# Kernel tuning notes

Measured on AMD Instinct MI355X. Metric: run time of the kernel, lower is better.

Reference implementation:

```python
import jax, jax.numpy as jnp
import numpy as np

NEG_BIG = -9e15
ALPHA = 0.2  # leakyrelu negative slope

N, F_IN, F_OUT = 8192, 512, 64


def setup_inputs() -> dict:
    key = jax.random.key(0)
    k1, k2, k3, k4 = jax.random.split(key, 4)
    input = jax.random.normal(k1, (N, F_IN), dtype=jnp.float32)
    adj = jax.random.randint(k2, (N, N), 0, 2, dtype=jnp.int32)
    W = jax.random.normal(k3, (F_IN, F_OUT), dtype=jnp.float32) * 0.05
    a = jax.random.normal(k4, (2 * F_OUT, 1), dtype=jnp.float32) * 0.1
    return {"input": input, "adj": adj, "W": W, "a": a}


def reference(input, adj, W, a):
    # h: [N, F_out]
    h = input @ W
    # The original builds a_input[i,j] = concat(h_i, h_j) and dots with a.
    # Decompose: e_ij = leakyrelu(h_i @ a_src + h_j @ a_dst) -- identical math,
    # avoids the N*N*2F intermediate.
    a_src = a[:F_OUT, 0]  # [F_out]
    a_dst = a[F_OUT:, 0]  # [F_out]
    s_src = h @ a_src     # [N]
    s_dst = h @ a_dst     # [N]
    e = jax.nn.leaky_relu(s_src[:, None] + s_dst[None, :], negative_slope=ALPHA)  # [N, N]
    masked = jnp.where(adj > 0, e, jnp.float32(NEG_BIG))
    attention = jax.nn.softmax(masked, axis=1)  # dropout omitted (eval mode)
    h_prime = attention @ h  # [N, F_out]
    return jax.nn.elu(h_prime)  # concat=True
```

## Files before the change

### kernel.cpp

```cpp
#include <hip/hip_runtime.h>
#include <hip/hip_bf16.h>

namespace {
constexpr int kN    = 8192;
constexpr int kFin  = 512;
constexpr int kFout = 64;
constexpr float kAlpha = 0.2f;
constexpr int kJSplit = 4;
constexpr int kJLen   = kN / kJSplit;
constexpr int kChunks = kJLen / 128;

using bf16x8 = __attribute__((ext_vector_type(8))) short;
using f32x4  = __attribute__((ext_vector_type(4))) float;

__device__ __forceinline__ unsigned short f2bf(float x) {
  return __builtin_bit_cast(unsigned short, __float2bfloat16(x));
}
__device__ __forceinline__ float lrelu(float x) {
  return fmaxf(x, kAlpha * x);
}
__device__ __forceinline__ unsigned int fkey(float x) {
  unsigned int b = __float_as_uint(x);
  return (b & 0x80000000u) ? ~b : (b | 0x80000000u);
}
__device__ __forceinline__ float fdec(unsigned int k) {
  return (k & 0x80000000u) ? __uint_as_float(k ^ 0x80000000u) : __uint_as_float(~k);
}
}

__global__ __launch_bounds__(256) void k_wt(const float* __restrict__ W,
                                            float* __restrict__ WT,
                                            unsigned int* __restrict__ Smax_u) {
  const int gid = blockIdx.x * 256 + threadIdx.x;
  if (gid == 0) *Smax_u = 0u;
  const int k = gid >> 6, f = gid & 63;
  WT[(size_t)f * kFin + k] = W[gid];
}

__global__ __launch_bounds__(256) void k_linear(
    const float* __restrict__ X, const float* __restrict__ WT, const float* __restrict__ A,
    unsigned short* __restrict__ hTf, float* __restrict__ s_src, float* __restrict__ s_dst,
    unsigned int* __restrict__ Smax_u)
{
  const int t = threadIdx.x;
  const int wv = t >> 6, f = t & 63;
  const int i0 = blockIdx.x * 16;

  __shared__ float Xlds[16 * kFin];
  __shared__ unsigned short h_sm[16][64];
  __shared__ float red[4];

  {
    const float4* Xg = (const float4*)(X + (size_t)i0 * kFin);
    float4* Xl = (float4*)Xlds;
    float4 v0 = Xg[t +   0], v1 = Xg[t + 256], v2 = Xg[t +  512], v3 = Xg[t +  768];
    float4 v4 = Xg[t +1024], v5 = Xg[t +1280], v6 = Xg[t + 1536], v7 = Xg[t + 1792];
    Xl[t +    0] = v0; Xl[t +  256] = v1; Xl[t +  512] = v2; Xl[t +  768] = v3;
    Xl[t + 1024] = v4; Xl[t + 1280] = v5; Xl[t + 1536] = v6; Xl[t + 1792] = v7;
  }
  __syncthreads();

  const int r0l = wv * 4;
  const float* w0 = WT + (size_t)f * kFin;
  float acc0 = 0.f, acc1 = 0.f, acc2 = 0.f, acc3 = 0.f;
  float4 wb0 = *(const float4*)(w0 + 0);
  float4 wb1 = *(const float4*)(w0 + 4);
  const float* xr = Xlds + r0l * kFin;
  for (int k = 0; k < kFin; k += 4) {
    const float4 wc = (k & 4) ? wb1 : wb0;
    if (k + 8 < kFin) {
      const float4 wn = *(const float4*)(w0 + k + 8);
      if (k & 4) wb1 = wn; else wb0 = wn;
    }
    const float4 xa = *(const float4*)(xr + k);
    const float4 xb = *(const float4*)(xr + kFin + k);
    const float4 xc = *(const float4*)(xr + 2 * kFin + k);
    const float4 xd = *(const float4*)(xr + 3 * kFin + k);
#pragma unroll
    for (int j = 0; j < 4; ++j) {
      const float wk = ((const float*)&wc)[j];
      acc0 = fmaf(((const float*)&xa)[j], wk, acc0);
      acc1 = fmaf(((const float*)&xb)[j], wk, acc1);
      acc2 = fmaf(((const float*)&xc)[j], wk, acc2);
      acc3 = fmaf(((const float*)&xd)[j], wk, acc3);
    }
  }

  const float asrc = A[f], adst = A[kFout + f];
  float accs[4] = {acc0, acc1, acc2, acc3};
  float dmax = -3.4e38f;
#pragma unroll
  for (int r = 0; r < 4; ++r) {
    float vs = accs[r] * asrc;
    float vd = accs[r] * adst;
#pragma unroll
    for (int off = 32; off > 0; off >>= 1) {
      vs += __shfl_xor(vs, off, 64);
      vd += __shfl_xor(vd, off, 64);
    }
    if (f == 0) {
      s_src[i0 + r0l + r] = vs;
      s_dst[i0 + r0l + r] = vd;
      dmax = fmaxf(dmax, vd);
    }
    h_sm[r0l + r][f] = f2bf(accs[r]);
  }
  if (f == 0) red[wv] = dmax;
  __syncthreads();
  if (t == 0) {
    float m = fmaxf(fmaxf(red[0], red[1]), fmaxf(red[2], red[3]));
    atomicMax(Smax_u, fkey(m));
  }

  if (t < 128) {
    const int jblk = i0 >> 5, half = (i0 >> 4) & 1;
    const int w = t >> 5, li = t & 31;
    const int lane = half * 32 + li;
    const int ql = li >> 4, fcol = w * 16 + (li & 15);
    bf16x8 v;
#pragma unroll
    for (int e = 0; e < 8; ++e) v[e] = (short)h_sm[ql * 8 + e][fcol];
    *(bf16x8*)(hTf + (size_t)jblk * 2048 + w * 512 + (size_t)lane * 8) = v;
  }
}

__global__ __launch_bounds__(256) void k_attn(
    const int* __restrict__ adj, const unsigned short* __restrict__ hTf,
    const float* __restrict__ s_src, const float* __restrict__ s_dst,
    const unsigned int* __restrict__ Smax_u, float* __restrict__ accp,
    float* __restrict__ lp)
{
  const int t = threadIdx.x;
  const int wv = t >> 6, lane = t & 63;
  const int b = blockIdx.x;
  const int i0 = (b >> 2) * 16;
  const int jbase = (b & 3) * kJLen;
  const int pr = t >> 4, jb = t & 15;

  __shared__ unsigned short Plds[2][16][136];

  const float S = fdec(*Smax_u);
  const float ssrc = s_src[i0 + pr];
  const float mr = lrelu(ssrc + S);

  float l_acc = 0.f;
  f32x4 acc = {0.f, 0.f, 0.f, 0.f};

  const int4*   aptr = (const int4*)(adj + (size_t)(i0 + pr) * kN + jbase + jb * 8);
  const float4* dptr = (const float4*)(s_dst + jbase + jb * 8);
  const unsigned short* hbase = hTf + (size_t)(jbase >> 5) * 2048 + wv * 512 + (size_t)lane * 8;

  const int mrow = lane & 15, quad = lane >> 4;

  int4   A0a = aptr[0],  A1a = aptr[1];
  float4 D0a = dptr[0],  D1a = dptr[1];
  int4   A0b = aptr[32], A1b = aptr[33];
  float4 D0b = dptr[32], D1b = dptr[33];

  auto phase = [&](int c, int sbuf, int4& A0, int4& A1, float4& D0, float4& D1)
      __attribute__((always_inline)) {
    float pv[8];
    {
      const int* aa = (const int*)&A0;
      const float* dd = (const float*)&D0;
#pragma unroll
      for (int j = 0; j < 4; ++j) {
        const float e = lrelu(ssrc + dd[j]);
        pv[j] = aa[j] > 0 ? __expf(e - mr) : 0.f;
      }
      aa = (const int*)&A1; dd = (const float*)&D1;
#pragma unroll
      for (int j = 0; j < 4; ++j) {
        const float e = lrelu(ssrc + dd[j]);
        pv[4 + j] = aa[j] > 0 ? __expf(e - mr) : 0.f;
      }
    }
    bf16x8 ps;
#pragma unroll
    for (int j = 0; j < 8; ++j) {
      l_acc += pv[j];
      ps[j] = (short)f2bf(pv[j]);
    }
    *(bf16x8*)&Plds[sbuf][pr][jb * 8] = ps;

    const uint4 hv0 = *(const uint4*)(hbase + (size_t)(c * 4 + 0) * 2048);
    const uint4 hv1 = *(const uint4*)(hbase + (size_t)(c * 4 + 1) * 2048);
    const uint4 hv2 = *(const uint4*)(hbase + (size_t)(c * 4 + 2) * 2048);
    const uint4 hv3 = *(const uint4*)(hbase + (size_t)(c * 4 + 3) * 2048);

    if (c + 2 < kChunks) {
      A0 = aptr[(c + 2) * 32]; A1 = aptr[(c + 2) * 32 + 1];
      D0 = dptr[(c + 2) * 32]; D1 = dptr[(c + 2) * 32 + 1];
    }
    __syncthreads();

    acc = __builtin_amdgcn_mfma_f32_16x16x32_bf16(
        *(const bf16x8*)&Plds[sbuf][mrow][0 * 32 + quad * 8], __builtin_bit_cast(bf16x8, hv0), acc, 0, 0, 0);
    acc = __builtin_amdgcn_mfma_f32_16x16x32_bf16(
        *(const bf16x8*)&Plds[sbuf][mrow][1 * 32 + quad * 8], __builtin_bit_cast(bf16x8, hv1), acc, 0, 0, 0);
    acc = __builtin_amdgcn_mfma_f32_16x16x32_bf16(
        *(const bf16x8*)&Plds[sbuf][mrow][2 * 32 + quad * 8], __builtin_bit_cast(bf16x8, hv2), acc, 0, 0, 0);
    acc = __builtin_amdgcn_mfma_f32_16x16x32_bf16(
        *(const bf16x8*)&Plds[sbuf][mrow][3 * 32 + quad * 8], __builtin_bit_cast(bf16x8, hv3), acc, 0, 0, 0);
  };

  for (int c = 0; c < kChunks; c += 2) {
    phase(c,     0, A0a, A1a, D0a, D1a);
    phase(c + 1, 1, A0b, A1b, D0b, D1b);
  }

  float lv = l_acc;
  lv += __shfl_xor(lv, 8, 64);
  lv += __shfl_xor(lv, 4, 64);
  lv += __shfl_xor(lv, 2, 64);
  lv += __shfl_xor(lv, 1, 64);
  if (jb == 0) lp[(size_t)b * 16 + pr] = lv;

  float* ab = accp + (size_t)b * 16 * 64;
#pragma unroll
  for (int reg = 0; reg < 4; ++reg) {
    ab[(quad * 4 + reg) * 64 + wv * 16 + mrow] = acc[reg];
  }
}

__global__ __launch_bounds__(256) void k_comb(const float* __restrict__ accp,
                                              const float* __restrict__ lp,
                                              float* __restrict__ out)
{
  const int gid = blockIdx.x * 256 + threadIdx.x;
  const int i = gid >> 6, f = gid & 63;
  const int ib = i >> 4, il = i & 15;
  const int b0 = ib * kJSplit;
  float a = 0.f, l = 0.f;
#pragma unroll
  for (int q = 0; q < kJSplit; ++q) {
    a += accp[((size_t)(b0 + q) * 16 + il) * 64 + f];
    l += lp[(size_t)(b0 + q) * 16 + il];
  }
  float v = a / l;
  v = v > 0.f ? v : __expf(v) - 1.f;
  out[gid] = v;
}

extern "C" void kernel_launch(void* const* d_in, const int* in_sizes, int n_in,
                              void* d_out, int out_size, void* d_ws, size_t ws_size,
                              hipStream_t stream) {
  const float* X   = (const float*)d_in[0];
  const int*   adj = (const int*)d_in[1];
  const float* W   = (const float*)d_in[2];
  const float* A   = (const float*)d_in[3];
  float* out = (float*)d_out;

  char* ws = (char*)d_ws;
  unsigned short* hTf = (unsigned short*)ws;  ws += (size_t)kN * kFout * 2;
  float* WT    = (float*)ws;                  ws += (size_t)kFout * kFin * 4;
  float* s_src = (float*)ws;                  ws += kN * 4;
  float* s_dst = (float*)ws;                  ws += kN * 4;
  unsigned int* Smax_u = (unsigned int*)ws;   ws += 256;
  float* accp  = (float*)ws;                  ws += (size_t)(kN / 16) * kJSplit * 16 * 64 * 4;
  float* lp    = (float*)ws;

  k_wt    <<<kFin * kFout / 256, 256, 0, stream>>>(W, WT, Smax_u);
  k_linear<<<kN / 16, 256, 0, stream>>>(X, WT, A, hTf, s_src, s_dst, Smax_u);
  k_attn  <<<(kN / 16) * kJSplit, 256, 0, stream>>>(adj, hTf, s_src, s_dst, Smax_u, accp, lp);
  k_comb  <<<kN * kFout / 256, 256, 0, stream>>>(accp, lp, out);
}
```

Before: 412.5 us.

## Feed MFMA A-operand from registers and split K across waves, dropping per-chunk LDS barrier

Each wave now computes its own probability fragment directly in the MFMA A-operand register layout and covers a separate 32-column slice of each 128-column chunk, accumulating all 64 output features in four accumulators. This removes the shared P tile, the LDS write/read round trip and the __syncthreads per chunk. A one-time cross-wave reduction through shared memory is added at the end, and each wave keeps more accumulator registers.

```diff
diff --git a/kernel.cpp b/kernel.cpp
--- a/kernel.cpp
+++ b/kernel.cpp
@@ -135,29 +135,29 @@
   const int b = blockIdx.x;
   const int i0 = (b >> 2) * 16;
   const int jbase = (b & 3) * kJLen;
-  const int pr = t >> 4, jb = t & 15;
-
-  __shared__ unsigned short Plds[2][16][136];
+  const int mrow = lane & 15, quad = lane >> 4;
+
+  __shared__ float Racc[4][16][64];
+  __shared__ float Rl[4][16];
 
   const float S = fdec(*Smax_u);
-  const float ssrc = s_src[i0 + pr];
+  const float ssrc = s_src[i0 + mrow];
   const float mr = lrelu(ssrc + S);
 
   float l_acc = 0.f;
-  f32x4 acc = {0.f, 0.f, 0.f, 0.f};
-
-  const int4*   aptr = (const int4*)(adj + (size_t)(i0 + pr) * kN + jbase + jb * 8);
-  const float4* dptr = (const float4*)(s_dst + jbase + jb * 8);
-  const unsigned short* hbase = hTf + (size_t)(jbase >> 5) * 2048 + wv * 512 + (size_t)lane * 8;
-
-  const int mrow = lane & 15, quad = lane >> 4;
+  f32x4 acc0 = {0.f,0.f,0.f,0.f}, acc1 = {0.f,0.f,0.f,0.f};
+  f32x4 acc2 = {0.f,0.f,0.f,0.f}, acc3 = {0.f,0.f,0.f,0.f};
+
+  const int4*   aptr = (const int4*)(adj + (size_t)(i0 + mrow) * kN + jbase + wv * 32 + quad * 8);
+  const float4* dptr = (const float4*)(s_dst + jbase + wv * 32 + quad * 8);
+  const unsigned short* hbase = hTf + ((size_t)(jbase >> 5) + wv) * 2048 + (size_t)lane * 8;
 
   int4   A0a = aptr[0],  A1a = aptr[1];
   float4 D0a = dptr[0],  D1a = dptr[1];
   int4   A0b = aptr[32], A1b = aptr[33];
   float4 D0b = dptr[32], D1b = dptr[33];
 
-  auto phase = [&](int c, int sbuf, int4& A0, int4& A1, float4& D0, float4& D1)
+  auto phase = [&](int c, int4& A0, int4& A1, float4& D0, float4& D1)
       __attribute__((always_inline)) {
     float pv[8];
     {
@@ -181,46 +181,51 @@
       l_acc += pv[j];
       ps[j] = (short)f2bf(pv[j]);
     }
-    *(bf16x8*)&Plds[sbuf][pr][jb * 8] = ps;
-
-    const uint4 hv0 = *(const uint4*)(hbase + (size_t)(c * 4 + 0) * 2048);
-    const uint4 hv1 = *(const uint4*)(hbase + (size_t)(c * 4 + 1) * 2048);
-    const uint4 hv2 = *(const uint4*)(hbase + (size_t)(c * 4 + 2) * 2048);
-    const uint4 hv3 = *(const uint4*)(hbase + (size_t)(c * 4 + 3) * 2048);
+
+    const unsigned short* hc = hbase + (size_t)c * 8192;
+    const uint4 hv0 = *(const uint4*)(hc + 0 * 512);
+    const uint4 hv1 = *(const uint4*)(hc + 1 * 512);
+    const uint4 hv2 = *(const uint4*)(hc + 2 * 512);
+    const uint4 hv3 = *(const uint4*)(hc + 3 * 512);
 
     if (c + 2 < kChunks) {
       A0 = aptr[(c + 2) * 32]; A1 = aptr[(c + 2) * 32 + 1];
       D0 = dptr[(c + 2) * 32]; D1 = dptr[(c + 2) * 32 + 1];
     }
-    __syncthreads();
-
-    acc = __builtin_amdgcn_mfma_f32_16x16x32_bf16(
-        *(const bf16x8*)&Plds[sbuf][mrow][0 * 32 + quad * 8], __builtin_bit_cast(bf16x8, hv0), acc, 0, 0, 0);
-    acc = __builtin_amdgcn_mfma_f32_16x16x32_bf16(
-        *(const bf16x8*)&Plds[sbuf][mrow][1 * 32 + quad * 8], __builtin_bit_cast(bf16x8, hv1), acc, 0, 0, 0);
-    acc = __builtin_amdgcn_mfma_f32_16x16x32_bf16(
-        *(const bf16x8*)&Plds[sbuf][mrow][2 * 32 + quad * 8], __builtin_bit_cast(bf16x8, hv2), acc, 0, 0, 0);
-    acc = __builtin_amdgcn_mfma_f32_16x16x32_bf16(
-        *(const bf16x8*)&Plds[sbuf][mrow][3 * 32 + quad * 8], __builtin_bit_cast(bf16x8, hv3), acc, 0, 0, 0);
+
+    acc0 = __builtin_amdgcn_mfma_f32_16x16x32_bf16(ps, __builtin_bit_cast(bf16x8, hv0), acc0, 0, 0, 0);
+    acc1 = __builtin_amdgcn_mfma_f32_16x16x32_bf16(ps, __builtin_bit_cast(bf16x8, hv1), acc1, 0, 0, 0);
+    acc2 = __builtin_amdgcn_mfma_f32_16x16x32_bf16(ps, __builtin_bit_cast(bf16x8, hv2), acc2, 0, 0, 0);
+    acc3 = __builtin_amdgcn_mfma_f32_16x16x32_bf16(ps, __builtin_bit_cast(bf16x8, hv3), acc3, 0, 0, 0);
   };
 
   for (int c = 0; c < kChunks; c += 2) {
-    phase(c,     0, A0a, A1a, D0a, D1a);
-    phase(c + 1, 1, A0b, A1b, D0b, D1b);
+    phase(c,     A0a, A1a, D0a, D1a);
+    phase(c + 1, A0b, A1b, D0b, D1b);
   }
 
   float lv = l_acc;
-  lv += __shfl_xor(lv, 8, 64);
-  lv += __shfl_xor(lv, 4, 64);
-  lv += __shfl_xor(lv, 2, 64);
-  lv += __shfl_xor(lv, 1, 64);
-  if (jb == 0) lp[(size_t)b * 16 + pr] = lv;
+  lv += __shfl_xor(lv, 16, 64);
+  lv += __shfl_xor(lv, 32, 64);
+  if (quad == 0) Rl[wv][mrow] = lv;
+
+#pragma unroll
+  for (int reg = 0; reg < 4; ++reg) {
+    Racc[wv][quad * 4 + reg][0 * 16 + mrow] = acc0[reg];
+    Racc[wv][quad * 4 + reg][1 * 16 + mrow] = acc1[reg];
+    Racc[wv][quad * 4 + reg][2 * 16 + mrow] = acc2[reg];
+    Racc[wv][quad * 4 + reg][3 * 16 + mrow] = acc3[reg];
+  }
+  __syncthreads();
 
   float* ab = accp + (size_t)b * 16 * 64;
-#pragma unroll
-  for (int reg = 0; reg < 4; ++reg) {
-    ab[(quad * 4 + reg) * 64 + wv * 16 + mrow] = acc[reg];
-  }
+  const int rr = t >> 4, ff = t & 15;
+#pragma unroll
+  for (int s = 0; s < 4; ++s) {
+    const int f = s * 16 + ff;
+    ab[rr * 64 + f] = Racc[0][rr][f] + Racc[1][rr][f] + Racc[2][rr][f] + Racc[3][rr][f];
+  }
+  if (t < 16) lp[(size_t)b * 16 + t] = Rl[0][t] + Rl[1][t] + Rl[2][t] + Rl[3][t];
 }
 
 __global__ __launch_bounds__(256) void k_comb(const float* __restrict__ accp,
```

New measurement: 423.5 us. +2.7%, slower.
